# Optimization experiments

Measured on AMD Instinct MI355X. Metric: run time of the kernel, lower is better.

Reference implementation:

```python
import jax, jax.numpy as jnp
import numpy as np
from jax import lax

# Fixed-point format: Q*.8 (8 fractional bits), as used by HGRNFixed8bit's
# to_fixed/from_fixed round-trip. We simulate it in float via round(x*256)/256.
FRAC = 256.0
EPS = 1e-5
B, T, D = 4, 2048, 2048  # batch, seq_len, hidden_size; input_dim = D (expand_ratio=1)


def to_fixed(x):
    return jnp.round(x * FRAC) / FRAC


def to_ternary(w):
    # BitNet-style ternarization: sign(w/mean|w|), zeroed where |w_norm| < 0.5
    scale = jnp.mean(jnp.abs(w))
    wn = w / (scale + 1e-5)
    t = jnp.sign(wn)
    return jnp.where(jnp.abs(wn) < 0.5, 0.0, t).astype(jnp.float32)


def per_channel_scale(w):
    # compute_scale: mean |w| over dim 0, stored in fixed point
    return to_fixed(jnp.mean(jnp.abs(w), axis=0))


def setup_inputs() -> dict:
    key = jax.random.key(0)
    ks = jax.random.split(key, 6)
    hidden_states = jax.random.normal(ks[0], (B, T, D), dtype=jnp.float32)
    # float master weights, then quantize exactly as quantize_weights() does
    w_i_f = jax.random.normal(ks[1], (D, D), dtype=jnp.float32) * 0.02  # i_proj.weight.T
    w_f_f = jax.random.normal(ks[2], (D, D), dtype=jnp.float32) * 0.02  # f_proj.weight.T
    w_g_f = jax.random.normal(ks[3], (D, D), dtype=jnp.float32) * 0.02  # g_proj.weight.T
    w_o_f = jax.random.normal(ks[4], (D, D), dtype=jnp.float32) * 0.02  # o_proj.weight [D_out, D_in]
    g_norm_w = jnp.ones((D,), dtype=jnp.float32)  # g_norm (RMSNorm-swish-gate) weight
    return {
        "hidden_states": hidden_states,
        "w_i": to_ternary(w_i_f), "w_f": to_ternary(w_f_f),
        "w_g": to_ternary(w_g_f), "w_o": to_ternary(w_o_f),
        "s_i": per_channel_scale(w_i_f), "s_f": per_channel_scale(w_f_f),
        "s_g": per_channel_scale(w_g_f), "s_o": per_channel_scale(w_o_f),
        "g_norm_w": g_norm_w,
    }


def reference(hidden_states, w_i, w_f, w_g, w_o, s_i, s_f, s_g, s_o, g_norm_w):
    # Quantize activations to 8-bit fixed point (to_fixed)
    x = to_fixed(hidden_states)                       # [B,T,D]
    # Ternary dequant-matmuls with per-channel scales
    i = jnp.einsum('btd,de->bte', x, w_i) * s_i       # input branch
    f = jax.nn.sigmoid(jnp.einsum('btd,de->bte', x, w_f) * s_f)  # forget gate
    g = jnp.einsum('btd,de->bte', x, w_g) * s_g       # output gate
    i = (1.0 - f) * i                                 # HGRN input gating
    # Gated linear recurrence h_t = f_t * h_{t-1} + i_t via associative scan
    def combine(a, b):
        af, ai = a
        bf, bi = b
        return (af * bf, ai * bf + bi)
    _, h = lax.associative_scan(combine, (f, i), axis=1)  # [B,T,E]
    # FusedRMSNormSwishGate: rmsnorm(h) * weight * swish(g)
    rms = h * lax.rsqrt(jnp.mean(h * h, axis=-1, keepdims=True) + EPS)
    o = rms * g_norm_w * (g * jax.nn.sigmoid(g))
    # Output ternary matmul (o_proj, weight untransposed -> use w_o.T),
    # per-input-channel scale, then from_fixed round-trip of the fixed output
    out = to_fixed(jnp.einsum('bte,oe->bto', o * s_o, w_o))  # [B,T,D]
    return out
```

## Files before the change

### kernel.cpp

```cpp
#include <hip/hip_runtime.h>
#include <hip/hip_bf16.h>
#include <stdint.h>
#include <math.h>


#define BATCH 4
#define SEQ   2048
#define DIM   2048
#define MROWS (BATCH*SEQ)
#define TCH   64
#define NCH   (SEQ/TCH)

#define GBM 256
#define GBN 256
#define GBK 64
#define GNT (DIM/GBK)
#define ASZ (GBM*GBK)
#define BSZ (GBN*GBK)

typedef unsigned short u16;
typedef __attribute__((ext_vector_type(8))) short short8;
typedef __attribute__((ext_vector_type(4))) float f32x4;

static __device__ __forceinline__ u16 f2bf_rne(float x) {
  uint32_t u = __float_as_uint(x);
  u += 0x7FFFu + ((u >> 16) & 1u);
  return (u16)(u >> 16);
}
static __device__ __forceinline__ float bf2f(u16 h) {
  return __uint_as_float(((uint32_t)h) << 16);
}

static __device__ __forceinline__ void gl2lds16(const void* g, void* l) {
  __builtin_amdgcn_global_load_lds((const __attribute__((address_space(1))) void*)g,
                                   (__attribute__((address_space(3))) void*)l,
                                   16, 0, 0);
}

__global__ __launch_bounds__(256) void diag_ws(float* __restrict__ out, float val) {
  size_t i = ((size_t)blockIdx.x * 256 + threadIdx.x) * 8;
#pragma unroll
  for (int j = 0; j < 8; j++) out[i + j] = val;
}

__global__ __launch_bounds__(256) void prep_x(const float* __restrict__ x,
                                              u16* __restrict__ XB) {
  size_t i = ((size_t)blockIdx.x * 256 + threadIdx.x) * 4;
  float4 v = *(const float4*)(x + i);
  float q[4] = {v.x, v.y, v.z, v.w};
  u16 hh[4];
#pragma unroll
  for (int j = 0; j < 4; j++) {
    float xq = rintf(q[j] * 256.0f) * 0.00390625f;
    hh[j] = f2bf_rne(xq);
  }
  *(uint2*)(XB + i) = make_uint2((uint32_t)hh[0] | ((uint32_t)hh[1] << 16),
                                 (uint32_t)hh[2] | ((uint32_t)hh[3] << 16));
}

__global__ void prep_wT(const float* __restrict__ w_i, const float* __restrict__ w_f,
                        const float* __restrict__ w_g, u16* __restrict__ WT) {
  __shared__ u16 tile[32][33];
  const int g = blockIdx.z;
  const float* __restrict__ w = (g == 0) ? w_i : (g == 1) ? w_f : w_g;
  u16* __restrict__ outp = WT + (size_t)g * DIM * DIM;
  const int d0 = blockIdx.x * 32;
  const int e0 = blockIdx.y * 32;
  const int tx = threadIdx.x;
  const int ty = threadIdx.y;
  for (int ii = ty; ii < 32; ii += 8)
    tile[ii][tx] = f2bf_rne(w[(size_t)(d0 + ii) * DIM + e0 + tx]);
  __syncthreads();
  for (int ii = ty; ii < 32; ii += 8)
    outp[(size_t)(e0 + ii) * DIM + d0 + tx] = tile[tx][ii];
}

__global__ __launch_bounds__(256) void prep_wo(const float* __restrict__ w, u16* __restrict__ WB) {
  size_t i = ((size_t)blockIdx.x * 256 + threadIdx.x) * 4;
  float4 v = *(const float4*)(w + i);
  *(uint2*)(WB + i) = make_uint2((uint32_t)f2bf_rne(v.x) | ((uint32_t)f2bf_rne(v.y) << 16),
                                 (uint32_t)f2bf_rne(v.z) | ((uint32_t)f2bf_rne(v.w) << 16));
}

static __device__ __forceinline__ void stage_tile(const u16* g, u16* buf, int tid) {
#pragma unroll
  for (int j = 0; j < 4; j++)
    gl2lds16(g + (size_t)j * (64 * DIM), buf + (size_t)(tid + j * 512) * 8);
}

static __device__ __forceinline__ void kloop256(const u16* __restrict__ Ag,
                                                const u16* __restrict__ Bg,
                                                u16* lds, f32x4 (&acc)[8][4]) {
  const int tid = threadIdx.x;
  const int lane16 = tid & 15;
  const int quad = (tid & 63) >> 4;
  const int wid = tid >> 6;
  const int waveM = wid >> 2;
  const int waveN = wid & 3;
  u16* ldsA = lds;
  u16* ldsB = lds + 2 * ASZ;

  const int rowS = tid >> 3;
  const int ccS = ((tid & 7) ^ (rowS & 7)) * 8;
  const u16* ga = Ag + (size_t)rowS * DIM + ccS;
  const u16* gb = Bg + (size_t)rowS * DIM + ccS;

  const int colx = (lane16 & 7) * 8;
  const int c0 = (quad * 8) ^ colx;
  const int c1 = (32 + quad * 8) ^ colx;
  const int arow = (waveM * 128 + lane16) * GBK;
  const int brow = (waveN * 64 + lane16) * GBK;

  stage_tile(ga, ldsA, tid);
  stage_tile(gb, ldsB, tid);
  asm volatile("s_waitcnt vmcnt(0)" ::: "memory");
  __builtin_amdgcn_s_barrier();

#pragma unroll 1
  for (int t = 0; t < GNT; ++t) {
    const u16* A = ldsA + (t & 1) * ASZ;
    const u16* B = ldsB + (t & 1) * BSZ;
    u16* SA = ldsA + ((t + 1) & 1) * ASZ;
    u16* SB = ldsB + ((t + 1) & 1) * BSZ;
    const bool pf = (t + 1 < GNT);

    if (pf) {
      stage_tile(ga + (size_t)(t + 1) * GBK, SA, tid);
      stage_tile(gb + (size_t)(t + 1) * GBK, SB, tid);
    }

    short8 bfr[4][2], afr[4][2];
#pragma unroll
    for (int ni = 0; ni < 4; ni++) {
      bfr[ni][0] = *(const short8*)(B + brow + ni * (16 * GBK) + c0);
      bfr[ni][1] = *(const short8*)(B + brow + ni * (16 * GBK) + c1);
    }
#pragma unroll
    for (int mi = 0; mi < 4; mi++) {
      afr[mi][0] = *(const short8*)(A + arow + mi * (16 * GBK) + c0);
      afr[mi][1] = *(const short8*)(A + arow + mi * (16 * GBK) + c1);
    }
    __builtin_amdgcn_s_setprio(1);
#pragma unroll
    for (int mi = 0; mi < 4; mi++)
#pragma unroll
      for (int ni = 0; ni < 4; ni++) {
        acc[mi][ni] = __builtin_amdgcn_mfma_f32_16x16x32_bf16(afr[mi][0], bfr[ni][0], acc[mi][ni], 0, 0, 0);
        acc[mi][ni] = __builtin_amdgcn_mfma_f32_16x16x32_bf16(afr[mi][1], bfr[ni][1], acc[mi][ni], 0, 0, 0);
      }
    __builtin_amdgcn_s_setprio(0);

#pragma unroll
    for (int mi = 0; mi < 4; mi++) {
      afr[mi][0] = *(const short8*)(A + arow + 64 * GBK + mi * (16 * GBK) + c0);
      afr[mi][1] = *(const short8*)(A + arow + 64 * GBK + mi * (16 * GBK) + c1);
    }
    __builtin_amdgcn_s_setprio(1);
#pragma unroll
    for (int mi = 0; mi < 4; mi++)
#pragma unroll
      for (int ni = 0; ni < 4; ni++) {
        acc[4 + mi][ni] = __builtin_amdgcn_mfma_f32_16x16x32_bf16(afr[mi][0], bfr[ni][0], acc[4 + mi][ni], 0, 0, 0);
        acc[4 + mi][ni] = __builtin_amdgcn_mfma_f32_16x16x32_bf16(afr[mi][1], bfr[ni][1], acc[4 + mi][ni], 0, 0, 0);
      }
    __builtin_amdgcn_s_setprio(0);

    if (pf) asm volatile("s_waitcnt vmcnt(0)" ::: "memory");
    __builtin_amdgcn_s_barrier();
  }
}

__global__ __launch_bounds__(512, 2) void gemm_gates8(
    const u16* __restrict__ XB, const u16* __restrict__ WT,
    const float* __restrict__ s_i, const float* __restrict__ s_f, const float* __restrict__ s_g,
    const float* __restrict__ gnw, const float* __restrict__ s_o,
    u16* __restrict__ Ib, u16* __restrict__ Fb, u16* __restrict__ Gb) {
  __shared__ __align__(16) u16 lds[2 * ASZ + 2 * BSZ];
  const int bid = blockIdx.x;
  const int i = (bid & 7) * 96 + (bid >> 3);
  const int gate = i >> 8;
  const int r = i & 255;
  const int m0 = (r & 31) * GBM;
  const int n0 = (r >> 5) * GBN;

  const u16* Ag = XB + (size_t)m0 * DIM;
  const u16* Bg = WT + (size_t)gate * DIM * DIM + (size_t)n0 * DIM;

  f32x4 acc[8][4];
#pragma unroll
  for (int a = 0; a < 8; a++)
#pragma unroll
    for (int b = 0; b < 4; b++) acc[a][b] = {0.f, 0.f, 0.f, 0.f};

  kloop256(Ag, Bg, lds, acc);

  __syncthreads();
  const int tid = threadIdx.x;
  const int lane16 = tid & 15;
  const int quad = (tid & 63) >> 4;
  const int wid = tid >> 6;
  const int waveM = wid >> 2;
  const int waveN = wid & 3;
  const float* __restrict__ sc = (gate == 0) ? s_i : (gate == 1) ? s_f : s_g;
  u16* __restrict__ Out = (gate == 0) ? Ib : (gate == 1) ? Fb : Gb;
  u16* T = lds;
#pragma unroll 1
  for (int p = 0; p < 2; ++p) {
    if ((waveN >> 1) == p) {
#pragma unroll
      for (int ni = 0; ni < 4; ni++) {
        const int n = n0 + waveN * 64 + ni * 16 + lane16;
        const float scale = sc[n];
        const float post = (gate == 2) ? gnw[n] * s_o[n] : 0.f;
        const int tcol = (waveN & 1) * 64 + ni * 16 + lane16;
#pragma unroll
        for (int a = 0; a < 8; a++) {
          const int lrow = waveM * 128 + (a >> 2) * 64 + (a & 3) * 16 + quad * 4;
#pragma unroll
          for (int r2 = 0; r2 < 4; r2++) {
            float v = acc[a][ni][r2] * scale;
            if (gate == 1) v = 1.0f / (1.0f + expf(-v));
            if (gate == 2) v = v / (1.0f + expf(-v)) * post;
            T[(lrow + r2) * 136 + tcol] = f2bf_rne(v);
          }
        }
      }
    }
    __syncthreads();
#pragma unroll
    for (int j = 0; j < 8; j++) {
      const int id = tid + j * 512;
      const int row = id >> 4;
      const int c16 = id & 15;
      uint4 v = *(const uint4*)(T + row * 136 + c16 * 8);
      *(uint4*)(Out + (size_t)(m0 + row) * DIM + n0 + p * 128 + c16 * 8) = v;
    }
    __syncthreads();
  }
}

__global__ __launch_bounds__(512, 2) void gemm_out8(const u16* __restrict__ OS,
                                                    const u16* __restrict__ WOB,
                                                    float* __restrict__ out) {
  __shared__ __align__(16) u16 lds[2 * ASZ + 2 * BSZ];
  const int bid = blockIdx.x;
  const int i = (bid & 7) * 32 + (bid >> 3);
  const int m0 = (i & 31) * GBM;
  const int n0 = (i >> 5) * GBN;

  const u16* Ag = OS + (size_t)m0 * DIM;
  const u16* Bg = WOB + (size_t)n0 * DIM;

  f32x4 acc[8][4];
#pragma unroll
  for (int a = 0; a < 8; a++)
#pragma unroll
    for (int b = 0; b < 4; b++) acc[a][b] = {0.f, 0.f, 0.f, 0.f};

  kloop256(Ag, Bg, lds, acc);

  const int tid = threadIdx.x;
  const int lane16 = tid & 15;
  const int quad = (tid & 63) >> 4;
  const int wid = tid >> 6;
  const int waveM = wid >> 2;
  const int waveN = wid & 3;
#pragma unroll
  for (int ni = 0; ni < 4; ni++) {
    const int n = n0 + waveN * 64 + ni * 16 + lane16;
#pragma unroll
    for (int a = 0; a < 8; a++) {
      const int mrow = m0 + waveM * 128 + (a >> 2) * 64 + (a & 3) * 16 + quad * 4;
#pragma unroll
      for (int r2 = 0; r2 < 4; r2++)
        out[(size_t)(mrow + r2) * DIM + n] = rintf(acc[a][ni][r2] * 256.0f) * 0.00390625f;
    }
  }
}

__global__ __launch_bounds__(256) void scan_phase1(const u16* __restrict__ Fb,
                                                   const u16* __restrict__ Ib,
                                                   float* __restrict__ Pc,
                                                   float* __restrict__ Sc) {
  const int e0 = (blockIdx.x * 256 + threadIdx.x) * 2;
  const int c = blockIdx.y;
  const int b = blockIdx.z;
  const size_t base = ((size_t)b * SEQ + (size_t)c * TCH) * DIM + e0;
  float P0 = 1.f, S0 = 0.f, P1 = 1.f, S1 = 0.f;
  for (int t = 0; t < TCH; t++) {
    const uint32_t fp = *(const uint32_t*)(Fb + base + (size_t)t * DIM);
    const uint32_t ip = *(const uint32_t*)(Ib + base + (size_t)t * DIM);
    const float f0 = bf2f((u16)fp), f1 = bf2f((u16)(fp >> 16));
    const float i0 = bf2f((u16)ip), i1 = bf2f((u16)(ip >> 16));
    S0 = S0 * f0 + (1.f - f0) * i0;  P0 *= f0;
    S1 = S1 * f1 + (1.f - f1) * i1;  P1 *= f1;
  }
  const size_t ci = ((size_t)b * NCH + c) * DIM + e0;
  *(float2*)(Pc + ci) = make_float2(P0, P1);
  *(float2*)(Sc + ci) = make_float2(S0, S1);
}

__global__ __launch_bounds__(256) void scan_phase2(const u16* __restrict__ Fb,
                                                   const u16* __restrict__ Ib,
                                                   const float* __restrict__ Pc,
                                                   const float* __restrict__ Sc,
                                                   u16* __restrict__ Hb) {
  const int e0 = (blockIdx.x * 256 + threadIdx.x) * 2;
  const int c = blockIdx.y;
  const int b = blockIdx.z;
  float h0 = 0.f, h1 = 0.f;
  for (int cc = 0; cc < c; cc++) {
    const size_t ci = ((size_t)b * NCH + cc) * DIM + e0;
    const float2 p = *(const float2*)(Pc + ci);
    const float2 s = *(const float2*)(Sc + ci);
    h0 = s.x + p.x * h0;
    h1 = s.y + p.y * h1;
  }
  const size_t base = ((size_t)b * SEQ + (size_t)c * TCH) * DIM + e0;
  for (int t = 0; t < TCH; t++) {
    const uint32_t fp = *(const uint32_t*)(Fb + base + (size_t)t * DIM);
    const uint32_t ip = *(const uint32_t*)(Ib + base + (size_t)t * DIM);
    const float f0 = bf2f((u16)fp), f1 = bf2f((u16)(fp >> 16));
    const float i0 = bf2f((u16)ip), i1 = bf2f((u16)(ip >> 16));
    h0 = f0 * h0 + (1.f - f0) * i0;
    h1 = f1 * h1 + (1.f - f1) * i1;
    *(uint32_t*)(Hb + base + (size_t)t * DIM) =
        (uint32_t)f2bf_rne(h0) | ((uint32_t)f2bf_rne(h1) << 16);
  }
}

__global__ __launch_bounds__(256) void rms_gate(const u16* __restrict__ Hb,
                                                const u16* __restrict__ SwGb,
                                                u16* __restrict__ OS) {
  const size_t base = (size_t)blockIdx.x * DIM;
  const int tid = threadIdx.x;
  const int e0 = tid * 8;
  uint4 hp = *(const uint4*)(Hb + base + e0);
  float hv[8];
  hv[0] = bf2f((u16)hp.x); hv[1] = bf2f((u16)(hp.x >> 16));
  hv[2] = bf2f((u16)hp.y); hv[3] = bf2f((u16)(hp.y >> 16));
  hv[4] = bf2f((u16)hp.z); hv[5] = bf2f((u16)(hp.z >> 16));
  hv[6] = bf2f((u16)hp.w); hv[7] = bf2f((u16)(hp.w >> 16));
  float ss = 0.f;
#pragma unroll
  for (int j = 0; j < 8; j++) ss += hv[j] * hv[j];
#pragma unroll
  for (int off = 32; off > 0; off >>= 1) ss += __shfl_down(ss, off, 64);
  __shared__ float red[4];
  if ((tid & 63) == 0) red[tid >> 6] = ss;
  __syncthreads();
  const float tot = red[0] + red[1] + red[2] + red[3];
  const float inv = 1.0f / sqrtf(tot * (1.0f / (float)DIM) + 1e-5f);

  uint4 gp = *(const uint4*)(SwGb + base + e0);
  float gv[8];
  gv[0] = bf2f((u16)gp.x); gv[1] = bf2f((u16)(gp.x >> 16));
  gv[2] = bf2f((u16)gp.y); gv[3] = bf2f((u16)(gp.y >> 16));
  gv[4] = bf2f((u16)gp.z); gv[5] = bf2f((u16)(gp.z >> 16));
  gv[6] = bf2f((u16)gp.w); gv[7] = bf2f((u16)(gp.w >> 16));
  u16 ov[8];
#pragma unroll
  for (int j = 0; j < 8; j++) ov[j] = f2bf_rne(hv[j] * inv * gv[j]);
  uint4 op;
  op.x = (uint32_t)ov[0] | ((uint32_t)ov[1] << 16);
  op.y = (uint32_t)ov[2] | ((uint32_t)ov[3] << 16);
  op.z = (uint32_t)ov[4] | ((uint32_t)ov[5] << 16);
  op.w = (uint32_t)ov[6] | ((uint32_t)ov[7] << 16);
  *(uint4*)(OS + base + e0) = op;
}

extern "C" void kernel_launch(void* const* d_in, const int* in_sizes, int n_in,
                              void* d_out, int out_size, void* d_ws, size_t ws_size,
                              hipStream_t stream) {
  (void)in_sizes; (void)n_in; (void)out_size;
  const float* x   = (const float*)d_in[0];
  const float* w_i = (const float*)d_in[1];
  const float* w_f = (const float*)d_in[2];
  const float* w_g = (const float*)d_in[3];
  const float* w_o = (const float*)d_in[4];
  const float* s_i = (const float*)d_in[5];
  const float* s_f = (const float*)d_in[6];
  const float* s_g = (const float*)d_in[7];
  const float* s_o = (const float*)d_in[8];
  const float* gnw = (const float*)d_in[9];
  float* out = (float*)d_out;

  const size_t MB = 1024 * 1024;
  const size_t NEED = 88 * MB;
  if (ws_size < NEED) {
    diag_ws<<<MROWS * DIM / 2048, 256, 0, stream>>>(out, (float)(ws_size / MB));
    return;
  }

  uint8_t* ws = (uint8_t*)d_ws;
  u16* XB = (u16*)(ws);
  u16* WT = (u16*)(ws + 32 * MB);
  u16* Ib = (u16*)(ws + 56 * MB);
  float* Pc = (float*)(ws + 32 * MB);
  float* Sc = (float*)(ws + 33 * MB);
  u16* WOB = (u16*)(ws + 34 * MB);
  u16* Hb  = XB;
  u16* OS  = Ib;
  u16* Gb = (u16*)d_out;
  u16* Fb = (u16*)((uint8_t*)d_out + 32 * MB);

  prep_x<<<MROWS * DIM / 1024, 256, 0, stream>>>(x, XB);
  prep_wT<<<dim3(DIM / 32, DIM / 32, 3), dim3(32, 8, 1), 0, stream>>>(w_i, w_f, w_g, WT);
  gemm_gates8<<<768, 512, 0, stream>>>(XB, WT, s_i, s_f, s_g, gnw, s_o, Ib, Fb, Gb);
  scan_phase1<<<dim3(DIM / 512, NCH, BATCH), 256, 0, stream>>>(Fb, Ib, Pc, Sc);
  scan_phase2<<<dim3(DIM / 512, NCH, BATCH), 256, 0, stream>>>(Fb, Ib, Pc, Sc, Hb);
  prep_wo<<<DIM * DIM / 1024, 256, 0, stream>>>(w_o, WOB);
  rms_gate<<<MROWS, 256, 0, stream>>>(Hb, Gb, OS);
  gemm_out8<<<256, 512, 0, stream>>>(OS, WOB, out);
}
```

Baseline: 560.9 us.

## Restructure GEMM k-loop into quadrant-staged half-tile pipeline with grouped block swizzle

Both GEMM kernels now split each 256x256 tile into four 128x128 quadrants, staging A and B in half-tiles interleaved with the MFMA phases. Partial vmcnt waits and extra barriers let global-to-LDS loads overlap compute instead of draining everything at the end of each k-step. Each wave now computes a 2x2 set of 64x32 sub-tiles, and the block-to-tile mapping groups four M tiles per N column to improve L2 reuse. This adds more barriers per iteration and more complex LDS slot management, which could cost sync overhead.

```diff
diff --git a/kernel.cpp b/kernel.cpp
--- a/kernel.cpp
+++ b/kernel.cpp
@@ -15,8 +15,8 @@
 #define GBN 256
 #define GBK 64
 #define GNT (DIM/GBK)
-#define ASZ (GBM*GBK)
-#define BSZ (GBN*GBK)
+#define HALF 8192
+#define SLOT (4*HALF)
 
 typedef unsigned short u16;
 typedef __attribute__((ext_vector_type(8))) short short8;
@@ -82,91 +82,127 @@
                                  (uint32_t)f2bf_rne(v.z) | ((uint32_t)f2bf_rne(v.w) << 16));
 }
 
-static __device__ __forceinline__ void stage_tile(const u16* g, u16* buf, int tid) {
-#pragma unroll
-  for (int j = 0; j < 4; j++)
-    gl2lds16(g + (size_t)j * (64 * DIM), buf + (size_t)(tid + j * 512) * 8);
+static __device__ __forceinline__ void stage_half(const u16* g, u16* l, int tid) {
+  gl2lds16(g, l + (size_t)tid * 8);
+  gl2lds16(g + (size_t)64 * DIM, l + (size_t)(tid + 512) * 8);
+}
+
+static __device__ __forceinline__ void read_a(short8 (&a)[4][2], const u16* base,
+                                              int aoff, int ck0, int ck1) {
+#pragma unroll
+  for (int mi = 0; mi < 4; mi++) {
+    a[mi][0] = *(const short8*)(base + aoff + mi * 1024 + ck0);
+    a[mi][1] = *(const short8*)(base + aoff + mi * 1024 + ck1);
+  }
+}
+static __device__ __forceinline__ void read_b(short8 (&b)[2][2], const u16* base,
+                                              int boff, int ck0, int ck1) {
+#pragma unroll
+  for (int ni = 0; ni < 2; ni++) {
+    b[ni][0] = *(const short8*)(base + boff + ni * 1024 + ck0);
+    b[ni][1] = *(const short8*)(base + boff + ni * 1024 + ck1);
+  }
+}
+static __device__ __forceinline__ void mfma_q(f32x4 (&accq)[4][2],
+                                              const short8 (&a)[4][2],
+                                              const short8 (&b)[2][2]) {
+  __builtin_amdgcn_s_setprio(1);
+#pragma unroll
+  for (int mi = 0; mi < 4; mi++)
+#pragma unroll
+    for (int ni = 0; ni < 2; ni++) {
+      accq[mi][ni] = __builtin_amdgcn_mfma_f32_16x16x32_bf16(a[mi][0], b[ni][0], accq[mi][ni], 0, 0, 0);
+      accq[mi][ni] = __builtin_amdgcn_mfma_f32_16x16x32_bf16(a[mi][1], b[ni][1], accq[mi][ni], 0, 0, 0);
+    }
+  __builtin_amdgcn_s_setprio(0);
 }
 
 static __device__ __forceinline__ void kloop256(const u16* __restrict__ Ag,
                                                 const u16* __restrict__ Bg,
-                                                u16* lds, f32x4 (&acc)[8][4]) {
+                                                u16* lds, f32x4 (&acc)[4][4][2]) {
   const int tid = threadIdx.x;
   const int lane16 = tid & 15;
   const int quad = (tid & 63) >> 4;
   const int wid = tid >> 6;
-  const int waveM = wid >> 2;
-  const int waveN = wid & 3;
-  u16* ldsA = lds;
-  u16* ldsB = lds + 2 * ASZ;
+  const int wRow = wid >> 2;
+  const int wCol = wid & 3;
 
   const int rowS = tid >> 3;
   const int ccS = ((tid & 7) ^ (rowS & 7)) * 8;
-  const u16* ga = Ag + (size_t)rowS * DIM + ccS;
-  const u16* gb = Bg + (size_t)rowS * DIM + ccS;
-
-  const int colx = (lane16 & 7) * 8;
-  const int c0 = (quad * 8) ^ colx;
-  const int c1 = (32 + quad * 8) ^ colx;
-  const int arow = (waveM * 128 + lane16) * GBK;
-  const int brow = (waveN * 64 + lane16) * GBK;
-
-  stage_tile(ga, ldsA, tid);
-  stage_tile(gb, ldsB, tid);
-  asm volatile("s_waitcnt vmcnt(0)" ::: "memory");
+  const u16* gA = Ag + (size_t)rowS * DIM + ccS;
+  const u16* gB = Bg + (size_t)rowS * DIM + ccS;
+  const size_t gH = (size_t)128 * DIM;
+
+  const int colx = lane16 & 7;
+  const int ck0 = (quad ^ colx) * 8;
+  const int ck1 = ((4 + quad) ^ colx) * 8;
+  const int aoff = (wRow * 64 + lane16) * 64;
+  const int boff = (wCol * 32 + lane16) * 64;
+
+  short8 a[4][2], bl[2][2], bh[2][2];
+
+  {
+    u16* s0 = lds;
+    stage_half(gA,      s0,            tid);
+    stage_half(gB,      s0 + 2 * HALF, tid);
+    stage_half(gB + gH, s0 + 3 * HALF, tid);
+    stage_half(gA + gH, s0 + 1 * HALF, tid);
+  }
+  asm volatile("s_waitcnt vmcnt(4)" ::: "memory");
   __builtin_amdgcn_s_barrier();
 
 #pragma unroll 1
-  for (int t = 0; t < GNT; ++t) {
-    const u16* A = ldsA + (t & 1) * ASZ;
-    const u16* B = ldsB + (t & 1) * BSZ;
-    u16* SA = ldsA + ((t + 1) & 1) * ASZ;
-    u16* SB = ldsB + ((t + 1) & 1) * BSZ;
-    const bool pf = (t + 1 < GNT);
-
-    if (pf) {
-      stage_tile(ga + (size_t)(t + 1) * GBK, SA, tid);
-      stage_tile(gb + (size_t)(t + 1) * GBK, SB, tid);
-    }
-
-    short8 bfr[4][2], afr[4][2];
-#pragma unroll
-    for (int ni = 0; ni < 4; ni++) {
-      bfr[ni][0] = *(const short8*)(B + brow + ni * (16 * GBK) + c0);
-      bfr[ni][1] = *(const short8*)(B + brow + ni * (16 * GBK) + c1);
-    }
-#pragma unroll
-    for (int mi = 0; mi < 4; mi++) {
-      afr[mi][0] = *(const short8*)(A + arow + mi * (16 * GBK) + c0);
-      afr[mi][1] = *(const short8*)(A + arow + mi * (16 * GBK) + c1);
-    }
-    __builtin_amdgcn_s_setprio(1);
-#pragma unroll
-    for (int mi = 0; mi < 4; mi++)
-#pragma unroll
-      for (int ni = 0; ni < 4; ni++) {
-        acc[mi][ni] = __builtin_amdgcn_mfma_f32_16x16x32_bf16(afr[mi][0], bfr[ni][0], acc[mi][ni], 0, 0, 0);
-        acc[mi][ni] = __builtin_amdgcn_mfma_f32_16x16x32_bf16(afr[mi][1], bfr[ni][1], acc[mi][ni], 0, 0, 0);
-      }
-    __builtin_amdgcn_s_setprio(0);
-
-#pragma unroll
-    for (int mi = 0; mi < 4; mi++) {
-      afr[mi][0] = *(const short8*)(A + arow + 64 * GBK + mi * (16 * GBK) + c0);
-      afr[mi][1] = *(const short8*)(A + arow + 64 * GBK + mi * (16 * GBK) + c1);
-    }
-    __builtin_amdgcn_s_setprio(1);
-#pragma unroll
-    for (int mi = 0; mi < 4; mi++)
-#pragma unroll
-      for (int ni = 0; ni < 4; ni++) {
-        acc[4 + mi][ni] = __builtin_amdgcn_mfma_f32_16x16x32_bf16(afr[mi][0], bfr[ni][0], acc[4 + mi][ni], 0, 0, 0);
-        acc[4 + mi][ni] = __builtin_amdgcn_mfma_f32_16x16x32_bf16(afr[mi][1], bfr[ni][1], acc[4 + mi][ni], 0, 0, 0);
-      }
-    __builtin_amdgcn_s_setprio(0);
-
-    if (pf) asm volatile("s_waitcnt vmcnt(0)" ::: "memory");
-    __builtin_amdgcn_s_barrier();
+  for (int t = 0; t < GNT - 1; ++t) {
+    const u16* S = lds + (t & 1) * SLOT;
+    u16* SN = lds + ((t + 1) & 1) * SLOT;
+    const size_t tg = (size_t)(t + 1) * GBK;
+
+    read_a(a, S, aoff, ck0, ck1);
+    read_b(bl, S + 2 * HALF, boff, ck0, ck1);
+    stage_half(gA + tg, SN, tid);
+    __builtin_amdgcn_s_barrier();
+    mfma_q(acc[0], a, bl);
+    asm volatile("s_waitcnt vmcnt(4)" ::: "memory");
+    __builtin_amdgcn_s_barrier();
+
+    read_b(bh, S + 3 * HALF, boff, ck0, ck1);
+    stage_half(gB + tg, SN + 2 * HALF, tid);
+    __builtin_amdgcn_s_barrier();
+    mfma_q(acc[1], a, bh);
+    asm volatile("s_waitcnt vmcnt(4)" ::: "memory");
+    __builtin_amdgcn_s_barrier();
+
+    read_a(a, S + HALF, aoff, ck0, ck1);
+    stage_half(gB + gH + tg, SN + 3 * HALF, tid);
+    __builtin_amdgcn_s_barrier();
+    mfma_q(acc[2], a, bl);
+    __builtin_amdgcn_s_barrier();
+
+    stage_half(gA + gH + tg, SN + 1 * HALF, tid);
+    __builtin_amdgcn_s_barrier();
+    mfma_q(acc[3], a, bh);
+    asm volatile("s_waitcnt vmcnt(4)" ::: "memory");
+    __builtin_amdgcn_s_barrier();
+  }
+
+  {
+    const u16* S = lds + ((GNT - 1) & 1) * SLOT;
+    read_a(a, S, aoff, ck0, ck1);
+    read_b(bl, S + 2 * HALF, boff, ck0, ck1);
+    __builtin_amdgcn_s_barrier();
+    mfma_q(acc[0], a, bl);
+    asm volatile("s_waitcnt vmcnt(2)" ::: "memory");
+    __builtin_amdgcn_s_barrier();
+    read_b(bh, S + 3 * HALF, boff, ck0, ck1);
+    __builtin_amdgcn_s_barrier();
+    mfma_q(acc[1], a, bh);
+    asm volatile("s_waitcnt vmcnt(0)" ::: "memory");
+    __builtin_amdgcn_s_barrier();
+    read_a(a, S + HALF, aoff, ck0, ck1);
+    __builtin_amdgcn_s_barrier();
+    mfma_q(acc[2], a, bl);
+    __builtin_amdgcn_s_barrier();
+    mfma_q(acc[3], a, bh);
   }
 }
 
@@ -175,22 +211,26 @@
     const float* __restrict__ s_i, const float* __restrict__ s_f, const float* __restrict__ s_g,
     const float* __restrict__ gnw, const float* __restrict__ s_o,
     u16* __restrict__ Ib, u16* __restrict__ Fb, u16* __restrict__ Gb) {
-  __shared__ __align__(16) u16 lds[2 * ASZ + 2 * BSZ];
+  __shared__ __align__(16) u16 lds[2 * SLOT];
   const int bid = blockIdx.x;
   const int i = (bid & 7) * 96 + (bid >> 3);
   const int gate = i >> 8;
   const int r = i & 255;
-  const int m0 = (r & 31) * GBM;
-  const int n0 = (r >> 5) * GBN;
+  const int sr = r >> 5;
+  const int s = r & 31;
+  const int m0 = (sr * 4 + (s & 3)) * GBM;
+  const int n0 = (s >> 2) * GBN;
 
   const u16* Ag = XB + (size_t)m0 * DIM;
   const u16* Bg = WT + (size_t)gate * DIM * DIM + (size_t)n0 * DIM;
 
-  f32x4 acc[8][4];
-#pragma unroll
-  for (int a = 0; a < 8; a++)
-#pragma unroll
-    for (int b = 0; b < 4; b++) acc[a][b] = {0.f, 0.f, 0.f, 0.f};
+  f32x4 acc[4][4][2];
+#pragma unroll
+  for (int q = 0; q < 4; q++)
+#pragma unroll
+    for (int a = 0; a < 4; a++)
+#pragma unroll
+      for (int b = 0; b < 2; b++) acc[q][a][b] = {0.f, 0.f, 0.f, 0.f};
 
   kloop256(Ag, Bg, lds, acc);
 
@@ -199,26 +239,28 @@
   const int lane16 = tid & 15;
   const int quad = (tid & 63) >> 4;
   const int wid = tid >> 6;
-  const int waveM = wid >> 2;
-  const int waveN = wid & 3;
+  const int wRow = wid >> 2;
+  const int wCol = wid & 3;
   const float* __restrict__ sc = (gate == 0) ? s_i : (gate == 1) ? s_f : s_g;
   u16* __restrict__ Out = (gate == 0) ? Ib : (gate == 1) ? Fb : Gb;
   u16* T = lds;
 #pragma unroll 1
   for (int p = 0; p < 2; ++p) {
-    if ((waveN >> 1) == p) {
-#pragma unroll
-      for (int ni = 0; ni < 4; ni++) {
-        const int n = n0 + waveN * 64 + ni * 16 + lane16;
+#pragma unroll
+    for (int hA = 0; hA < 2; ++hA) {
+      const int q = hA * 2 + p;
+#pragma unroll
+      for (int ni = 0; ni < 2; ++ni) {
+        const int tcol = wCol * 32 + ni * 16 + lane16;
+        const int n = n0 + p * 128 + tcol;
         const float scale = sc[n];
         const float post = (gate == 2) ? gnw[n] * s_o[n] : 0.f;
-        const int tcol = (waveN & 1) * 64 + ni * 16 + lane16;
-#pragma unroll
-        for (int a = 0; a < 8; a++) {
-          const int lrow = waveM * 128 + (a >> 2) * 64 + (a & 3) * 16 + quad * 4;
-#pragma unroll
-          for (int r2 = 0; r2 < 4; r2++) {
-            float v = acc[a][ni][r2] * scale;
+#pragma unroll
+        for (int mi = 0; mi < 4; ++mi) {
+          const int lrow = hA * 128 + wRow * 64 + mi * 16 + quad * 4;
+#pragma unroll
+          for (int r2 = 0; r2 < 4; ++r2) {
+            float v = acc[q][mi][ni][r2] * scale;
             if (gate == 1) v = 1.0f / (1.0f + expf(-v));
             if (gate == 2) v = v / (1.0f + expf(-v)) * post;
             T[(lrow + r2) * 136 + tcol] = f2bf_rne(v);
@@ -242,20 +284,22 @@
 __global__ __launch_bounds__(512, 2) void gemm_out8(const u16* __restrict__ OS,
                                                     const u16* __restrict__ WOB,
                                                     float* __restrict__ out) {
-  __shared__ __align__(16) u16 lds[2 * ASZ + 2 * BSZ];
+  __shared__ __align__(16) u16 lds[2 * SLOT];
   const int bid = blockIdx.x;
-  const int i = (bid & 7) * 32 + (bid >> 3);
-  const int m0 = (i & 31) * GBM;
-  const int n0 = (i >> 5) * GBN;
+  const int l = bid >> 3;
+  const int m0 = ((bid & 7) * 4 + (l & 3)) * GBM;
+  const int n0 = (l >> 2) * GBN;
 
   const u16* Ag = OS + (size_t)m0 * DIM;
   const u16* Bg = WOB + (size_t)n0 * DIM;
 
-  f32x4 acc[8][4];
-#pragma unroll
-  for (int a = 0; a < 8; a++)
-#pragma unroll
-    for (int b = 0; b < 4; b++) acc[a][b] = {0.f, 0.f, 0.f, 0.f};
+  f32x4 acc[4][4][2];
+#pragma unroll
+  for (int q = 0; q < 4; q++)
+#pragma unroll
+    for (int a = 0; a < 4; a++)
+#pragma unroll
+      for (int b = 0; b < 2; b++) acc[q][a][b] = {0.f, 0.f, 0.f, 0.f};
 
   kloop256(Ag, Bg, lds, acc);
 
@@ -263,17 +307,20 @@
   const int lane16 = tid & 15;
   const int quad = (tid & 63) >> 4;
   const int wid = tid >> 6;
-  const int waveM = wid >> 2;
-  const int waveN = wid & 3;
-#pragma unroll
-  for (int ni = 0; ni < 4; ni++) {
-    const int n = n0 + waveN * 64 + ni * 16 + lane16;
-#pragma unroll
-    for (int a = 0; a < 8; a++) {
-      const int mrow = m0 + waveM * 128 + (a >> 2) * 64 + (a & 3) * 16 + quad * 4;
-#pragma unroll
-      for (int r2 = 0; r2 < 4; r2++)
-        out[(size_t)(mrow + r2) * DIM + n] = rintf(acc[a][ni][r2] * 256.0f) * 0.00390625f;
+  const int wRow = wid >> 2;
+  const int wCol = wid & 3;
+#pragma unroll
+  for (int q = 0; q < 4; ++q) {
+#pragma unroll
+    for (int ni = 0; ni < 2; ++ni) {
+      const int n = n0 + (q & 1) * 128 + wCol * 32 + ni * 16 + lane16;
+#pragma unroll
+      for (int mi = 0; mi < 4; ++mi) {
+        const int mrow = m0 + (q >> 1) * 128 + wRow * 64 + mi * 16 + quad * 4;
+#pragma unroll
+        for (int r2 = 0; r2 < 4; ++r2)
+          out[(size_t)(mrow + r2) * DIM + n] = rintf(acc[q][mi][ni][r2] * 256.0f) * 0.00390625f;
+      }
     }
   }
 }
```

After: 575.2 us. 2.5% more time.

## Split GEMM tile staging into half-tiles with finer-grained prefetch waits

Applied to the files above, without the earlier changes.

The shared GEMM k-loop now stages each 256x64 A/B tile as two 128-row halves and interleaves their prefetch with the two MFMA phases, using partial vmcnt waits and mid-iteration barriers instead of one full wait at the end of each step. The wave-to-tile mapping changes to interleaved 64-row/32-column quadrants, and both GEMMs' epilogues are remapped to match. Block-index swizzles are also changed to group M tiles in fours for better L2 reuse. The goal is to hide global-to-LDS latency better, at the cost of extra barriers and more delicate synchronisation.

```diff
diff --git a/kernel.cpp b/kernel.cpp
--- a/kernel.cpp
+++ b/kernel.cpp
@@ -15,8 +15,8 @@
 #define GBN 256
 #define GBK 64
 #define GNT (DIM/GBK)
-#define ASZ (GBM*GBK)
-#define BSZ (GBN*GBK)
+#define HALF 8192
+#define SLOT (4*HALF)
 
 typedef unsigned short u16;
 typedef __attribute__((ext_vector_type(8))) short short8;
@@ -82,10 +82,9 @@
                                  (uint32_t)f2bf_rne(v.z) | ((uint32_t)f2bf_rne(v.w) << 16));
 }
 
-static __device__ __forceinline__ void stage_tile(const u16* g, u16* buf, int tid) {
-#pragma unroll
-  for (int j = 0; j < 4; j++)
-    gl2lds16(g + (size_t)j * (64 * DIM), buf + (size_t)(tid + j * 512) * 8);
+static __device__ __forceinline__ void stage_half(const u16* g, u16* l, int tid) {
+  gl2lds16(g, l + (size_t)tid * 8);
+  gl2lds16(g + (size_t)64 * DIM, l + (size_t)(tid + 512) * 8);
 }
 
 static __device__ __forceinline__ void kloop256(const u16* __restrict__ Ag,
@@ -95,78 +94,88 @@
   const int lane16 = tid & 15;
   const int quad = (tid & 63) >> 4;
   const int wid = tid >> 6;
-  const int waveM = wid >> 2;
-  const int waveN = wid & 3;
-  u16* ldsA = lds;
-  u16* ldsB = lds + 2 * ASZ;
+  const int wR = wid >> 2;
+  const int wC = wid & 3;
 
   const int rowS = tid >> 3;
   const int ccS = ((tid & 7) ^ (rowS & 7)) * 8;
-  const u16* ga = Ag + (size_t)rowS * DIM + ccS;
-  const u16* gb = Bg + (size_t)rowS * DIM + ccS;
-
-  const int colx = (lane16 & 7) * 8;
-  const int c0 = (quad * 8) ^ colx;
-  const int c1 = (32 + quad * 8) ^ colx;
-  const int arow = (waveM * 128 + lane16) * GBK;
-  const int brow = (waveN * 64 + lane16) * GBK;
-
-  stage_tile(ga, ldsA, tid);
-  stage_tile(gb, ldsB, tid);
-  asm volatile("s_waitcnt vmcnt(0)" ::: "memory");
+  const u16* gA = Ag + (size_t)rowS * DIM + ccS;
+  const u16* gB = Bg + (size_t)rowS * DIM + ccS;
+  const size_t gH = (size_t)128 * DIM;
+
+  const int cswz = lane16 & 7;
+  const int ck0 = (quad ^ cswz) * 8;
+  const int ck1 = ((4 + quad) ^ cswz) * 8;
+  const int arow = (wR * 64 + lane16) * 64;
+  const int brow = (wC * 32 + lane16) * 64;
+
+  stage_half(gA,      lds + 0 * HALF, tid);
+  stage_half(gB,      lds + 2 * HALF, tid);
+  stage_half(gB + gH, lds + 3 * HALF, tid);
+  stage_half(gA + gH, lds + 1 * HALF, tid);
+  asm volatile("s_waitcnt vmcnt(2)" ::: "memory");
   __builtin_amdgcn_s_barrier();
+
+  short8 af[4][2], bfr[4][2];
 
 #pragma unroll 1
   for (int t = 0; t < GNT; ++t) {
-    const u16* A = ldsA + (t & 1) * ASZ;
-    const u16* B = ldsB + (t & 1) * BSZ;
-    u16* SA = ldsA + ((t + 1) & 1) * ASZ;
-    u16* SB = ldsB + ((t + 1) & 1) * BSZ;
+    const u16* S = lds + (t & 1) * SLOT;
+    u16* SN = lds + ((t + 1) & 1) * SLOT;
     const bool pf = (t + 1 < GNT);
-
+    const size_t tg = (size_t)(t + 1) * GBK;
+
+#pragma unroll
+    for (int j = 0; j < 4; j++) {
+      const u16* bb = S + 2 * HALF + (j >> 1) * HALF + brow + (j & 1) * 1024;
+      bfr[j][0] = *(const short8*)(bb + ck0);
+      bfr[j][1] = *(const short8*)(bb + ck1);
+    }
+#pragma unroll
+    for (int mi = 0; mi < 4; mi++) {
+      const u16* aa = S + arow + mi * 1024;
+      af[mi][0] = *(const short8*)(aa + ck0);
+      af[mi][1] = *(const short8*)(aa + ck1);
+    }
     if (pf) {
-      stage_tile(ga + (size_t)(t + 1) * GBK, SA, tid);
-      stage_tile(gb + (size_t)(t + 1) * GBK, SB, tid);
-    }
-
-    short8 bfr[4][2], afr[4][2];
-#pragma unroll
-    for (int ni = 0; ni < 4; ni++) {
-      bfr[ni][0] = *(const short8*)(B + brow + ni * (16 * GBK) + c0);
-      bfr[ni][1] = *(const short8*)(B + brow + ni * (16 * GBK) + c1);
-    }
-#pragma unroll
-    for (int mi = 0; mi < 4; mi++) {
-      afr[mi][0] = *(const short8*)(A + arow + mi * (16 * GBK) + c0);
-      afr[mi][1] = *(const short8*)(A + arow + mi * (16 * GBK) + c1);
-    }
+      stage_half(gA + tg, SN + 0 * HALF, tid);
+      stage_half(gB + tg, SN + 2 * HALF, tid);
+      asm volatile("s_waitcnt vmcnt(4)" ::: "memory");
+    } else {
+      asm volatile("s_waitcnt vmcnt(0)" ::: "memory");
+    }
+    __builtin_amdgcn_s_barrier();
     __builtin_amdgcn_s_setprio(1);
 #pragma unroll
     for (int mi = 0; mi < 4; mi++)
 #pragma unroll
-      for (int ni = 0; ni < 4; ni++) {
-        acc[mi][ni] = __builtin_amdgcn_mfma_f32_16x16x32_bf16(afr[mi][0], bfr[ni][0], acc[mi][ni], 0, 0, 0);
-        acc[mi][ni] = __builtin_amdgcn_mfma_f32_16x16x32_bf16(afr[mi][1], bfr[ni][1], acc[mi][ni], 0, 0, 0);
+      for (int j = 0; j < 4; j++) {
+        acc[mi][j] = __builtin_amdgcn_mfma_f32_16x16x32_bf16(af[mi][0], bfr[j][0], acc[mi][j], 0, 0, 0);
+        acc[mi][j] = __builtin_amdgcn_mfma_f32_16x16x32_bf16(af[mi][1], bfr[j][1], acc[mi][j], 0, 0, 0);
       }
     __builtin_amdgcn_s_setprio(0);
 
 #pragma unroll
     for (int mi = 0; mi < 4; mi++) {
-      afr[mi][0] = *(const short8*)(A + arow + 64 * GBK + mi * (16 * GBK) + c0);
-      afr[mi][1] = *(const short8*)(A + arow + 64 * GBK + mi * (16 * GBK) + c1);
+      const u16* aa = S + HALF + arow + mi * 1024;
+      af[mi][0] = *(const short8*)(aa + ck0);
+      af[mi][1] = *(const short8*)(aa + ck1);
+    }
+    if (pf) {
+      stage_half(gB + gH + tg, SN + 3 * HALF, tid);
+      stage_half(gA + gH + tg, SN + 1 * HALF, tid);
+      asm volatile("s_waitcnt vmcnt(2)" ::: "memory");
+      __builtin_amdgcn_s_barrier();
     }
     __builtin_amdgcn_s_setprio(1);
 #pragma unroll
     for (int mi = 0; mi < 4; mi++)
 #pragma unroll
-      for (int ni = 0; ni < 4; ni++) {
-        acc[4 + mi][ni] = __builtin_amdgcn_mfma_f32_16x16x32_bf16(afr[mi][0], bfr[ni][0], acc[4 + mi][ni], 0, 0, 0);
-        acc[4 + mi][ni] = __builtin_amdgcn_mfma_f32_16x16x32_bf16(afr[mi][1], bfr[ni][1], acc[4 + mi][ni], 0, 0, 0);
+      for (int j = 0; j < 4; j++) {
+        acc[4 + mi][j] = __builtin_amdgcn_mfma_f32_16x16x32_bf16(af[mi][0], bfr[j][0], acc[4 + mi][j], 0, 0, 0);
+        acc[4 + mi][j] = __builtin_amdgcn_mfma_f32_16x16x32_bf16(af[mi][1], bfr[j][1], acc[4 + mi][j], 0, 0, 0);
       }
     __builtin_amdgcn_s_setprio(0);
-
-    if (pf) asm volatile("s_waitcnt vmcnt(0)" ::: "memory");
-    __builtin_amdgcn_s_barrier();
   }
 }
 
@@ -175,13 +184,15 @@
     const float* __restrict__ s_i, const float* __restrict__ s_f, const float* __restrict__ s_g,
     const float* __restrict__ gnw, const float* __restrict__ s_o,
     u16* __restrict__ Ib, u16* __restrict__ Fb, u16* __restrict__ Gb) {
-  __shared__ __align__(16) u16 lds[2 * ASZ + 2 * BSZ];
+  __shared__ __align__(16) u16 lds[2 * SLOT];
   const int bid = blockIdx.x;
   const int i = (bid & 7) * 96 + (bid >> 3);
   const int gate = i >> 8;
   const int r = i & 255;
-  const int m0 = (r & 31) * GBM;
-  const int n0 = (r >> 5) * GBN;
+  const int sr = r >> 5;
+  const int s = r & 31;
+  const int m0 = (sr * 4 + (s & 3)) * GBM;
+  const int n0 = (s >> 2) * GBN;
 
   const u16* Ag = XB + (size_t)m0 * DIM;
   const u16* Bg = WT + (size_t)gate * DIM * DIM + (size_t)n0 * DIM;
@@ -199,32 +210,32 @@
   const int lane16 = tid & 15;
   const int quad = (tid & 63) >> 4;
   const int wid = tid >> 6;
-  const int waveM = wid >> 2;
-  const int waveN = wid & 3;
+  const int wR = wid >> 2;
+  const int wC = wid & 3;
   const float* __restrict__ sc = (gate == 0) ? s_i : (gate == 1) ? s_f : s_g;
   u16* __restrict__ Out = (gate == 0) ? Ib : (gate == 1) ? Fb : Gb;
   u16* T = lds;
-#pragma unroll 1
+#pragma unroll
   for (int p = 0; p < 2; ++p) {
-    if ((waveN >> 1) == p) {
-#pragma unroll
-      for (int ni = 0; ni < 4; ni++) {
-        const int n = n0 + waveN * 64 + ni * 16 + lane16;
-        const float scale = sc[n];
-        const float post = (gate == 2) ? gnw[n] * s_o[n] : 0.f;
-        const int tcol = (waveN & 1) * 64 + ni * 16 + lane16;
-#pragma unroll
-        for (int a = 0; a < 8; a++) {
-          const int lrow = waveM * 128 + (a >> 2) * 64 + (a & 3) * 16 + quad * 4;
-#pragma unroll
-          for (int r2 = 0; r2 < 4; r2++) {
-            float v = acc[a][ni][r2] * scale;
+#pragma unroll
+    for (int ni = 0; ni < 2; ++ni) {
+      const int tcol = wC * 32 + ni * 16 + lane16;
+      const int n = n0 + p * 128 + tcol;
+      const float scale = sc[n];
+      const float post = (gate == 2) ? gnw[n] * s_o[n] : 0.f;
+#pragma unroll
+      for (int hA = 0; hA < 2; ++hA)
+#pragma unroll
+        for (int mi = 0; mi < 4; ++mi) {
+          const int lrow = hA * 128 + wR * 64 + mi * 16 + quad * 4;
+#pragma unroll
+          for (int r2 = 0; r2 < 4; ++r2) {
+            float v = acc[hA * 4 + mi][p * 2 + ni][r2] * scale;
             if (gate == 1) v = 1.0f / (1.0f + expf(-v));
             if (gate == 2) v = v / (1.0f + expf(-v)) * post;
             T[(lrow + r2) * 136 + tcol] = f2bf_rne(v);
           }
         }
-      }
     }
     __syncthreads();
 #pragma unroll
@@ -242,11 +253,11 @@
 __global__ __launch_bounds__(512, 2) void gemm_out8(const u16* __restrict__ OS,
                                                     const u16* __restrict__ WOB,
                                                     float* __restrict__ out) {
-  __shared__ __align__(16) u16 lds[2 * ASZ + 2 * BSZ];
+  __shared__ __align__(16) u16 lds[2 * SLOT];
   const int bid = blockIdx.x;
-  const int i = (bid & 7) * 32 + (bid >> 3);
-  const int m0 = (i & 31) * GBM;
-  const int n0 = (i >> 5) * GBN;
+  const int l = bid >> 3;
+  const int m0 = ((bid & 7) * 4 + (l & 3)) * GBM;
+  const int n0 = (l >> 2) * GBN;
 
   const u16* Ag = OS + (size_t)m0 * DIM;
   const u16* Bg = WOB + (size_t)n0 * DIM;
@@ -263,19 +274,24 @@
   const int lane16 = tid & 15;
   const int quad = (tid & 63) >> 4;
   const int wid = tid >> 6;
-  const int waveM = wid >> 2;
-  const int waveN = wid & 3;
-#pragma unroll
-  for (int ni = 0; ni < 4; ni++) {
-    const int n = n0 + waveN * 64 + ni * 16 + lane16;
-#pragma unroll
-    for (int a = 0; a < 8; a++) {
-      const int mrow = m0 + waveM * 128 + (a >> 2) * 64 + (a & 3) * 16 + quad * 4;
-#pragma unroll
-      for (int r2 = 0; r2 < 4; r2++)
-        out[(size_t)(mrow + r2) * DIM + n] = rintf(acc[a][ni][r2] * 256.0f) * 0.00390625f;
-    }
-  }
+  const int wR = wid >> 2;
+  const int wC = wid & 3;
+#pragma unroll
+  for (int p = 0; p < 2; ++p)
+#pragma unroll
+    for (int ni = 0; ni < 2; ++ni) {
+      const int n = n0 + p * 128 + wC * 32 + ni * 16 + lane16;
+#pragma unroll
+      for (int hA = 0; hA < 2; ++hA)
+#pragma unroll
+        for (int mi = 0; mi < 4; ++mi) {
+          const int mrow = m0 + hA * 128 + wR * 64 + mi * 16 + quad * 4;
+#pragma unroll
+          for (int r2 = 0; r2 < 4; ++r2)
+            out[(size_t)(mrow + r2) * DIM + n] =
+                rintf(acc[hA * 4 + mi][p * 2 + ni][r2] * 256.0f) * 0.00390625f;
+        }
+    }
 }
 
 __global__ __launch_bounds__(256) void scan_phase1(const u16* __restrict__ Fb,
```

After: 512.2 us. -8.7%, faster.
